# Performance work log

Measured on AMD Instinct MI355X. Metric: run time of the kernel, lower is better.

## Reference

```python
import jax, jax.numpy as jnp
import numpy as np

NUM_HEADS = 8
KEY_DIM = 32      # head_dim * attention_ratio = 64 * 0.5
HEAD_DIM = 64     # in_channels // num_heads = 512 // 8
SCALE = KEY_DIM ** -0.5


def _bn(y, g, b):
    # eval-mode BatchNorm2d with running_mean=0, running_var=1 -> per-channel affine
    return y * g[:, None, None] + b[:, None, None]


def setup_inputs() -> dict:
    key = jax.random.key(0)
    ks = jax.random.split(key, 4)
    B, C, H, W = 16, 512, 32, 32
    qkv_ch = C + 2 * NUM_HEADS * KEY_DIM  # 1024
    return {
        "x": jax.random.normal(ks[0], (B, C, H, W), jnp.float32),
        "w_qkv": jax.random.normal(ks[1], (qkv_ch, C), jnp.float32) * 0.02,
        "g_qkv": jnp.ones((qkv_ch,), jnp.float32),
        "b_qkv": jnp.zeros((qkv_ch,), jnp.float32),
        "w_pos": jax.random.normal(ks[2], (C, 1, 3, 3), jnp.float32) * 0.1,
        "g_pos": jnp.ones((C,), jnp.float32),
        "b_pos": jnp.zeros((C,), jnp.float32),
        "w_out": jax.random.normal(ks[3], (C, C), jnp.float32) * 0.02,
        "g_out": jnp.ones((C,), jnp.float32),
        "b_out": jnp.zeros((C,), jnp.float32),
    }


def reference(x, w_qkv, g_qkv, b_qkv, w_pos, g_pos, b_pos, w_out, g_out, b_out):
    B, C, H, W = x.shape
    HW = H * W
    # 1x1 conv QKV projection + BN (no activation)
    qkv = _bn(jnp.einsum('bchw,oc->bohw', x, w_qkv), g_qkv, b_qkv)
    # b (heads * (2*kd + hd)) h w -> b heads (2*kd + hd) hw
    qkv = qkv.reshape(B, NUM_HEADS, 2 * KEY_DIM + HEAD_DIM, HW)
    q = qkv[:, :, :KEY_DIM]                      # [B, h, kd, HW]
    k = qkv[:, :, KEY_DIM:2 * KEY_DIM]           # [B, h, kd, HW]
    v = qkv[:, :, 2 * KEY_DIM:]                  # [B, h, hd, HW]
    # attention scores: q^T k, scaled
    scores = jnp.einsum('bhdn,bhdm->bhnm', q, k) * SCALE   # [B, h, HW, HW]
    weights = jax.nn.softmax(scores, axis=-1)
    # attended = v @ weights^T : [B, h, hd, HW]
    attended = jnp.einsum('bhdm,bhnm->bhdn', v, weights)
    attended = attended.reshape(B, C, H, W)
    # positional encoding: depthwise 3x3 conv on value, + BN
    v_spatial = v.reshape(B, C, H, W)
    pos = jax.lax.conv_general_dilated(
        v_spatial, w_pos, window_strides=(1, 1), padding='SAME',
        feature_group_count=C, dimension_numbers=('NCHW', 'OIHW', 'NCHW'))
    pos = _bn(pos, g_pos, b_pos)
    enhanced = attended + pos
    # 1x1 output projection + BN
    return _bn(jnp.einsum('bchw,oc->bohw', enhanced, w_out), g_out, b_out)
```

## Files before the change

### kernel.cpp

```cpp
#include <hip/hip_runtime.h>
#include <hip/hip_bf16.h>
#include <stdint.h>

#define NHEADS 8
#define KDIM   32
#define HDIM   64
#define CDIM   512
#define HWN    1024
#define BATCH  16
#define QKVCH  1024
#define SCALE_F 0.17677669529663687f
#define QSCALE_F (0.17677669529663687f * 1.44269504088896341f)

typedef __attribute__((ext_vector_type(8))) short short8;
typedef __attribute__((ext_vector_type(4))) float f32x4;

static __device__ __forceinline__ unsigned short f2bf(float f) {
    unsigned int u = __float_as_uint(f);
    unsigned int r = (u + 0x7fffu + ((u >> 16) & 1u)) >> 16;
    return (unsigned short)r;
}
static __device__ __forceinline__ float bf2f(unsigned short h) {
    return __uint_as_float(((unsigned int)h) << 16);
}
static __device__ __forceinline__ unsigned int cvtpk(float a, float b) {
    unsigned int r;
    asm("v_cvt_pk_bf16_f32 %0, %1, %2" : "=v"(r) : "v"(a), "v"(b));
    return r;
}
static __device__ __forceinline__ float fexp2(float x) {
    float r;
    asm("v_exp_f32 %0, %1" : "=v"(r) : "v"(x));
    return r;
}
static __device__ __forceinline__ float bfelem(const uint4& v, int j) {
    unsigned int w = ((j >> 1) == 0) ? v.x : ((j >> 1) == 1) ? v.y : ((j >> 1) == 2) ? v.z : v.w;
    return (j & 1) ? __uint_as_float(w & 0xffff0000u) : __uint_as_float(w << 16);
}
static __device__ __forceinline__ unsigned int addpk(unsigned int a, unsigned int p) {
    float lo = __uint_as_float(a << 16) + __uint_as_float(p << 16);
    float hi = __uint_as_float(a & 0xffff0000u) + __uint_as_float(p & 0xffff0000u);
    return cvtpk(lo, hi);
}

static __device__ __forceinline__ void gload_lds16(const void* g, void* l) {
    __builtin_amdgcn_global_load_lds(
        (const __attribute__((address_space(1))) void*)g,
        (__attribute__((address_space(3))) void*)l, 16, 0, 0);
}

__global__ __launch_bounds__(256) void convert_kernel(const float* __restrict__ src,
                                                      unsigned short* __restrict__ dst, int n) {
    int i = (blockIdx.x * 256 + threadIdx.x) * 8;
    if (i >= n) return;
    float4 a = *(const float4*)(src + i);
    float4 c = *(const float4*)(src + i + 4);
    unsigned short r[8] __attribute__((aligned(16))) =
        {f2bf(a.x), f2bf(a.y), f2bf(a.z), f2bf(a.w), f2bf(c.x), f2bf(c.y), f2bf(c.z), f2bf(c.w)};
    *(uint4*)(dst + i) = *(const uint4*)r;
}

__global__ __launch_bounds__(256) void transpose_kernel(const float* __restrict__ x,
                                                        unsigned short* __restrict__ xt) {
    __shared__ unsigned short tl[64][66];
    int bid = blockIdx.x;
    int b = bid >> 7, ct = (bid >> 4) & 7, nt = bid & 15;
    int t = threadIdx.x;
#pragma unroll
    for (int i = 0; i < 16; ++i) {
        int idx = i * 256 + t;
        int cl = idx >> 6, nl = idx & 63;
        tl[cl][nl] = f2bf(x[((size_t)(b * CDIM + ct * 64 + cl)) * HWN + nt * 64 + nl]);
    }
    __syncthreads();
    int a8 = (t & 7) * 8;
    int nl = t >> 3;
#pragma unroll
    for (int i = 0; i < 2; ++i) {
        int n = nt * 64 + nl + 32 * i;
        unsigned short tmp[8] __attribute__((aligned(16)));
#pragma unroll
        for (int j = 0; j < 8; ++j) tmp[j] = tl[a8 + j][nl + 32 * i];
        *(uint4*)(xt + ((size_t)b * HWN + n) * CDIM + ct * 64 + a8) = *(const uint4*)tmp;
    }
}

template <int MODE>
__global__ __launch_bounds__(256) void gemm_bf16(
    const unsigned short* __restrict__ A, const unsigned short* __restrict__ Bt,
    const float* __restrict__ gvec, const float* __restrict__ bvec,
    void* out0, void* out1, void* out2, int Mtiles) {
    __shared__ unsigned short lds[2][128][32];
    int bid = blockIdx.x;
    int b  = bid / (Mtiles * 8);
    int rmn = bid % (Mtiles * 8);
    int mt = rmn >> 3, nt = rmn & 7;
    int t = threadIdx.x, lane = t & 63, w = t >> 6, g = lane >> 4, lr = lane & 15;
    int M0 = mt * 128, N0 = nt * 128;
    const unsigned short* Ab = A + (size_t)M0 * 512;
    const unsigned short* Bb = Bt + (size_t)b * HWN * 512 + (size_t)N0 * 512;
    int rw = (w >> 1) * 64, cw = (w & 1) * 64;

    f32x4 acc[4][4] = {};
    for (int k0 = 0; k0 < 512; k0 += 32) {
#pragma unroll
        for (int p = 0; p < 2; ++p) {
            int row = (p * 4 + w) * 16 + lr;
            int slot = lane >> 4;
            gload_lds16(Ab + row * 512 + k0 + slot * 8,
                        (char*)&lds[0][0][0] + (p * 4 + w) * 1024);
            gload_lds16(Bb + row * 512 + k0 + slot * 8,
                        (char*)&lds[1][0][0] + (p * 4 + w) * 1024);
        }
        __syncthreads();
        const char* Abase = (const char*)&lds[0][0][0] + lane * 16;
        const char* Bbase = (const char*)&lds[1][0][0] + lane * 16;
        short8 af[4], bfr[4];
#pragma unroll
        for (int i = 0; i < 4; ++i) {
            af[i]  = *(const short8*)(Abase + ((rw >> 4) + i) * 1024);
            bfr[i] = *(const short8*)(Bbase + ((cw >> 4) + i) * 1024);
        }
#pragma unroll
        for (int i = 0; i < 4; ++i)
#pragma unroll
            for (int j = 0; j < 4; ++j)
                acc[i][j] = __builtin_amdgcn_mfma_f32_16x16x32_bf16(af[i], bfr[j], acc[i][j], 0, 0, 0);
        __syncthreads();
    }

#pragma unroll
    for (int i = 0; i < 4; ++i) {
        int obase = M0 + rw + i * 16 + g * 4;
#pragma unroll
        for (int j = 0; j < 4; ++j) {
            int n = N0 + cw + j * 16 + lr;
            float val[4];
#pragma unroll
            for (int rr = 0; rr < 4; ++rr) {
                int o = obase + rr;
                val[rr] = acc[i][j][rr] * gvec[o] + bvec[o];
            }
            if (MODE == 0) {
                int h = obase >> 7, jj = obase & 127;
                size_t bh = (size_t)((b << 3) + h);
                if (jj < 32) {
                    uint2 pk = {cvtpk(val[0] * QSCALE_F, val[1] * QSCALE_F),
                                cvtpk(val[2] * QSCALE_F, val[3] * QSCALE_F)};
                    *(uint2*)((unsigned short*)out0 + (bh * HWN + n) * KDIM + jj) = pk;
                } else if (jj < 64) {
                    uint2 pk = {cvtpk(val[0], val[1]), cvtpk(val[2], val[3])};
                    *(uint2*)((unsigned short*)out1 + (bh * HWN + n) * KDIM + (jj - 32)) = pk;
                } else {
#pragma unroll
                    for (int rr = 0; rr < 4; ++rr)
                        ((unsigned short*)out2)[(bh * HDIM + (jj - 64 + rr)) * HWN + n] = f2bf(val[rr]);
                }
            } else {
#pragma unroll
                for (int rr = 0; rr < 4; ++rr)
                    ((float*)out0)[((size_t)(b * CDIM + obase + rr)) * HWN + n] = val[rr];
            }
        }
    }
}

__global__ __launch_bounds__(256) void attn_kernel(
    const unsigned short* __restrict__ qw, const unsigned short* __restrict__ kw,
    const unsigned short* __restrict__ vw, unsigned short* __restrict__ attw) {
    __shared__ unsigned short kt[2][128 * 32];
    __shared__ unsigned short vt[2][64 * 128];
    int p = blockIdx.x;
    int bh = ((p >> 6) << 3) | (p & 7);
    int ntile = (p >> 3) & 7;
    int b = bh >> 3, h = bh & 7;
    int t = threadIdx.x, lane = t & 63, w = t >> 6, g = lane >> 4, lr = lane & 15;
    int N0 = ntile * 128 + w * 32;
    const unsigned short* qb = qw + (size_t)bh * HWN * KDIM;
    const unsigned short* kb = kw + (size_t)bh * HWN * KDIM;
    const unsigned short* vb = vw + (size_t)bh * HDIM * HWN;

    short8 qf0 = *(const short8*)(qb + (size_t)(N0 + lr) * KDIM + g * 8);
    short8 qf1 = *(const short8*)(qb + (size_t)(N0 + 16 + lr) * KDIM + g * 8);
    f32x4 acc0[4] = {}, acc1[4] = {};
    f32x4 zero = {0.f, 0.f, 0.f, 0.f};
    float l0 = 0.f, l1 = 0.f;
    int sw = (lr & 7) << 4;
    int g8 = g << 3;

    auto stage = [&](int mt, int buf) {
        int M0 = mt * 128;
#pragma unroll
        for (int pp = 0; pp < 2; ++pp) {
            int s = pp * 256 + w * 64 + lane;
            int row = (s >> 7) * 32 + ((s >> 6) & 1) * 16 + lr;
            gload_lds16(kb + (size_t)(M0 + row) * KDIM + g * 8,
                        (char*)kt[buf] + (pp * 4 + w) * 1024);
        }
#pragma unroll
        for (int pp = 0; pp < 4; ++pp) {
            int s = pp * 256 + w * 64 + lane;
            int dd = s >> 4, u = s & 15;
            gload_lds16(vb + (size_t)dd * HWN + M0 + ((u ^ (dd & 7)) << 3),
                        (char*)vt[buf] + (pp * 4 + w) * 1024);
        }
    };

    stage(0, 0);
    __syncthreads();
    for (int mt = 0; mt < 8; ++mt) {
        int cur = mt & 1;
        if (mt < 7) stage(mt + 1, cur ^ 1);
        const char* ktc = (const char*)kt[cur] + lane * 16;
        const char* vrow = (const char*)vt[cur] + lr * 256;
#pragma unroll
        for (int mc = 0; mc < 4; ++mc) {
            short8 kf0 = *(const short8*)(ktc + mc * 2048);
            short8 kf1 = *(const short8*)(ktc + mc * 2048 + 1024);
            f32x4 s00 = __builtin_amdgcn_mfma_f32_16x16x32_bf16(kf0, qf0, zero, 0, 0, 0);
            f32x4 s01 = __builtin_amdgcn_mfma_f32_16x16x32_bf16(kf1, qf0, zero, 0, 0, 0);
            f32x4 s10 = __builtin_amdgcn_mfma_f32_16x16x32_bf16(kf0, qf1, zero, 0, 0, 0);
            f32x4 s11 = __builtin_amdgcn_mfma_f32_16x16x32_bf16(kf1, qf1, zero, 0, 0, 0);
            float e0[8], e1[8];
#pragma unroll
            for (int i = 0; i < 4; ++i) {
                e0[i] = fexp2(s00[i]); e0[4 + i] = fexp2(s01[i]);
                e1[i] = fexp2(s10[i]); e1[4 + i] = fexp2(s11[i]);
            }
            l0 += ((e0[0] + e0[1]) + (e0[2] + e0[3])) + ((e0[4] + e0[5]) + (e0[6] + e0[7]));
            l1 += ((e1[0] + e1[1]) + (e1[2] + e1[3])) + ((e1[4] + e1[5]) + (e1[6] + e1[7]));
            union { uint4 u; short8 s; } pf0, pf1;
            pf0.u = (uint4){cvtpk(e0[0], e0[1]), cvtpk(e0[2], e0[3]),
                            cvtpk(e0[4], e0[5]), cvtpk(e0[6], e0[7])};
            pf1.u = (uint4){cvtpk(e1[0], e1[1]), cvtpk(e1[2], e1[3]),
                            cvtpk(e1[4], e1[5]), cvtpk(e1[6], e1[7])};
            int off0 = (mc * 64 + g8) ^ sw;
            int off1 = off0 ^ 32;
#pragma unroll
            for (int dt = 0; dt < 4; ++dt) {
                uint2 v0 = *(const uint2*)(vrow + dt * 4096 + off0);
                uint2 v1 = *(const uint2*)(vrow + dt * 4096 + off1);
                union { uint2 u[2]; short8 s; } vf;
                vf.u[0] = v0; vf.u[1] = v1;
                acc0[dt] = __builtin_amdgcn_mfma_f32_16x16x32_bf16(vf.s, pf0.s, acc0[dt], 0, 0, 0);
                acc1[dt] = __builtin_amdgcn_mfma_f32_16x16x32_bf16(vf.s, pf1.s, acc1[dt], 0, 0, 0);
            }
        }
        __syncthreads();
    }
    l0 += __shfl_xor(l0, 16); l0 += __shfl_xor(l0, 32);
    l1 += __shfl_xor(l1, 16); l1 += __shfl_xor(l1, 32);
    float inv0 = 1.0f / l0, inv1 = 1.0f / l1;
    size_t robase = ((size_t)b * HWN + N0 + lr) * CDIM + h * HDIM + g * 4;
#pragma unroll
    for (int dt = 0; dt < 4; ++dt) {
        uint2 o0 = {cvtpk(acc0[dt][0] * inv0, acc0[dt][1] * inv0),
                    cvtpk(acc0[dt][2] * inv0, acc0[dt][3] * inv0)};
        uint2 o1 = {cvtpk(acc1[dt][0] * inv1, acc1[dt][1] * inv1),
                    cvtpk(acc1[dt][2] * inv1, acc1[dt][3] * inv1)};
        *(uint2*)(attw + robase + dt * 16) = o0;
        *(uint2*)(attw + robase + 16 * CDIM + dt * 16) = o1;
    }
}

__global__ __launch_bounds__(256) void conv_kernel(
    const unsigned short* __restrict__ vw,
    const float* __restrict__ wpos, const float* __restrict__ gpos, const float* __restrict__ bpos,
    const unsigned short* __restrict__ attw,
    unsigned short* __restrict__ ew) {
    __shared__ unsigned short po[32][520];
    int bid = blockIdx.x;
    int b = bid >> 5, y = bid & 31;
    int t = threadIdx.x;
#pragma unroll
    for (int hh = 0; hh < 2; ++hh) {
        int c = hh * 256 + t;
        const unsigned short* vrow = vw + ((size_t)(b * CDIM + c)) * HWN;
        uint4 rv[3][4];
#pragma unroll
        for (int dy = 0; dy < 3; ++dy) {
            int r = y + dy - 1;
            bool ok = (r >= 0) && (r < 32);
#pragma unroll
            for (int s2 = 0; s2 < 4; ++s2) {
                uint4 z = {0u, 0u, 0u, 0u};
                rv[dy][s2] = ok ? *(const uint4*)(vrow + r * 32 + s2 * 8) : z;
            }
        }
        float wreg[9];
#pragma unroll
        for (int k = 0; k < 9; ++k) wreg[k] = wpos[c * 9 + k];
        float gc = gpos[c], bc = bpos[c];
#pragma unroll
        for (int x = 0; x < 32; ++x) {
            float sum = 0.f;
#pragma unroll
            for (int dy = 0; dy < 3; ++dy)
#pragma unroll
                for (int dx = 0; dx < 3; ++dx) {
                    int xx = x + dx - 1;
                    if (xx >= 0 && xx < 32)
                        sum += wreg[dy * 3 + dx] * bfelem(rv[dy][xx >> 3], xx & 7);
                }
            po[x][c] = f2bf(sum * gc + bc);
        }
    }
    __syncthreads();
    int c8 = (t & 63) * 8;
    int xg = t >> 6;
#pragma unroll
    for (int i = 0; i < 8; ++i) {
        int x = xg + i * 4;
        size_t nidx = ((size_t)b * HWN + y * 32 + x) * CDIM + c8;
        uint4 a = *(const uint4*)(attw + nidx);
        uint4 p = *(const uint4*)(&po[x][c8]);
        uint4 o = {addpk(a.x, p.x), addpk(a.y, p.y), addpk(a.z, p.z), addpk(a.w, p.w)};
        *(uint4*)(ew + nidx) = o;
    }
}

extern "C" void kernel_launch(void* const* d_in, const int* in_sizes, int n_in,
                              void* d_out, int out_size, void* d_ws, size_t ws_size,
                              hipStream_t stream) {
    const float* x     = (const float*)d_in[0];
    const float* w_qkv = (const float*)d_in[1];
    const float* g_qkv = (const float*)d_in[2];
    const float* b_qkv = (const float*)d_in[3];
    const float* w_pos = (const float*)d_in[4];
    const float* g_pos = (const float*)d_in[5];
    const float* b_pos = (const float*)d_in[6];
    const float* w_out = (const float*)d_in[7];
    const float* g_out = (const float*)d_in[8];
    const float* b_out = (const float*)d_in[9];
    char* ws = (char*)d_ws;
    unsigned short* xt   = (unsigned short*)(ws);
    unsigned short* wqb  = (unsigned short*)(ws + 16777216);
    unsigned short* wob  = (unsigned short*)(ws + 17825792);
    unsigned short* qw   = (unsigned short*)(ws + 18350080);
    unsigned short* kw   = (unsigned short*)(ws + 26738688);
    unsigned short* vw   = (unsigned short*)(ws + 35127296);
    unsigned short* attw = (unsigned short*)(ws + 51904512);

    convert_kernel<<<256, 256, 0, stream>>>(w_qkv, wqb, QKVCH * CDIM);
    convert_kernel<<<128, 256, 0, stream>>>(w_out, wob, CDIM * CDIM);
    transpose_kernel<<<2048, 256, 0, stream>>>(x, xt);
    gemm_bf16<0><<<1024, 256, 0, stream>>>(wqb, xt, g_qkv, b_qkv, qw, kw, vw, 8);
    attn_kernel<<<1024, 256, 0, stream>>>(qw, kw, vw, attw);
    conv_kernel<<<512, 256, 0, stream>>>(vw, w_pos, g_pos, b_pos, attw, xt );
    gemm_bf16<1><<<512, 256, 0, stream>>>(wob, xt , g_out, b_out, d_out, nullptr, nullptr, 4);
}
```

Before: 162.5 us.

## Load GEMM fragments directly from global with register double-buffering and XCD-aware block mapping

After: 194.0 us. 1.19x slower.

```diff
diff --git a/kernel.cpp b/kernel.cpp
--- a/kernel.cpp
+++ b/kernel.cpp
@@ -85,48 +85,59 @@
     }
 }
 
-template <int MODE>
+template <int MODE, int MT>
 __global__ __launch_bounds__(256) void gemm_bf16(
     const unsigned short* __restrict__ A, const unsigned short* __restrict__ Bt,
     const float* __restrict__ gvec, const float* __restrict__ bvec,
-    void* out0, void* out1, void* out2, int Mtiles) {
-    __shared__ unsigned short lds[2][128][32];
-    int bid = blockIdx.x;
-    int b  = bid / (Mtiles * 8);
-    int rmn = bid % (Mtiles * 8);
-    int mt = rmn >> 3, nt = rmn & 7;
+    void* out0, void* out1, void* out2) {
+    constexpr int BPB = MT * 8;
+    int p = blockIdx.x;
+    int xcd = p & 7;
+    int r = p >> 3;
+    int hi = (r >= BPB) ? 1 : 0;
+    int b = xcd * 2 + hi;
+    int idx = r - hi * BPB;
+    int mt = idx >> 3, nt = idx & 7;
     int t = threadIdx.x, lane = t & 63, w = t >> 6, g = lane >> 4, lr = lane & 15;
     int M0 = mt * 128, N0 = nt * 128;
-    const unsigned short* Ab = A + (size_t)M0 * 512;
-    const unsigned short* Bb = Bt + (size_t)b * HWN * 512 + (size_t)N0 * 512;
     int rw = (w >> 1) * 64, cw = (w & 1) * 64;
 
+    const unsigned short* Ap = A + (size_t)(M0 + rw + lr) * 512 + g * 8;
+    const unsigned short* Bp = Bt + (size_t)b * HWN * 512 + (size_t)(N0 + cw + lr) * 512 + g * 8;
+
     f32x4 acc[4][4] = {};
-    for (int k0 = 0; k0 < 512; k0 += 32) {
-#pragma unroll
-        for (int p = 0; p < 2; ++p) {
-            int row = (p * 4 + w) * 16 + lr;
-            int slot = lane >> 4;
-            gload_lds16(Ab + row * 512 + k0 + slot * 8,
-                        (char*)&lds[0][0][0] + (p * 4 + w) * 1024);
-            gload_lds16(Bb + row * 512 + k0 + slot * 8,
-                        (char*)&lds[1][0][0] + (p * 4 + w) * 1024);
-        }
-        __syncthreads();
-        const char* Abase = (const char*)&lds[0][0][0] + lane * 16;
-        const char* Bbase = (const char*)&lds[1][0][0] + lane * 16;
-        short8 af[4], bfr[4];
-#pragma unroll
-        for (int i = 0; i < 4; ++i) {
-            af[i]  = *(const short8*)(Abase + ((rw >> 4) + i) * 1024);
-            bfr[i] = *(const short8*)(Bbase + ((cw >> 4) + i) * 1024);
+    short8 a0[4], b0[4], a1[4], b1[4];
+#pragma unroll
+    for (int i = 0; i < 4; ++i) {
+        a0[i] = *(const short8*)(Ap + i * 8192);
+        b0[i] = *(const short8*)(Bp + i * 8192);
+    }
+#pragma unroll
+    for (int ks = 0; ks < 16; ks += 2) {
+        if (ks + 1 < 16) {
+#pragma unroll
+            for (int i = 0; i < 4; ++i) {
+                a1[i] = *(const short8*)(Ap + i * 8192 + (ks + 1) * 32);
+                b1[i] = *(const short8*)(Bp + i * 8192 + (ks + 1) * 32);
+            }
         }
 #pragma unroll
         for (int i = 0; i < 4; ++i)
 #pragma unroll
             for (int j = 0; j < 4; ++j)
-                acc[i][j] = __builtin_amdgcn_mfma_f32_16x16x32_bf16(af[i], bfr[j], acc[i][j], 0, 0, 0);
-        __syncthreads();
+                acc[i][j] = __builtin_amdgcn_mfma_f32_16x16x32_bf16(a0[i], b0[j], acc[i][j], 0, 0, 0);
+        if (ks + 2 < 16) {
+#pragma unroll
+            for (int i = 0; i < 4; ++i) {
+                a0[i] = *(const short8*)(Ap + i * 8192 + (ks + 2) * 32);
+                b0[i] = *(const short8*)(Bp + i * 8192 + (ks + 2) * 32);
+            }
+        }
+#pragma unroll
+        for (int i = 0; i < 4; ++i)
+#pragma unroll
+            for (int j = 0; j < 4; ++j)
+                acc[i][j] = __builtin_amdgcn_mfma_f32_16x16x32_bf16(a1[i], b1[j], acc[i][j], 0, 0, 0);
     }
 
 #pragma unroll
@@ -344,8 +355,8 @@
     convert_kernel<<<256, 256, 0, stream>>>(w_qkv, wqb, QKVCH * CDIM);
     convert_kernel<<<128, 256, 0, stream>>>(w_out, wob, CDIM * CDIM);
     transpose_kernel<<<2048, 256, 0, stream>>>(x, xt);
-    gemm_bf16<0><<<1024, 256, 0, stream>>>(wqb, xt, g_qkv, b_qkv, qw, kw, vw, 8);
+    gemm_bf16<0, 8><<<1024, 256, 0, stream>>>(wqb, xt, g_qkv, b_qkv, qw, kw, vw);
     attn_kernel<<<1024, 256, 0, stream>>>(qw, kw, vw, attw);
     conv_kernel<<<512, 256, 0, stream>>>(vw, w_pos, g_pos, b_pos, attw, xt );
-    gemm_bf16<1><<<512, 256, 0, stream>>>(wob, xt , g_out, b_out, d_out, nullptr, nullptr, 4);
-}
+    gemm_bf16<1, 4><<<512, 256, 0, stream>>>(wob, xt , g_out, b_out, d_out, nullptr, nullptr);
+}
```

## Enlarge GEMM tiles, double-buffer LDS with K=64 stages, and XCD-aware block mapping

Applied to the files above, without the earlier changes.

After: 141.7 us. 1.15x faster.

```diff
diff --git a/kernel.cpp b/kernel.cpp
--- a/kernel.cpp
+++ b/kernel.cpp
@@ -85,56 +85,84 @@
     }
 }
 
-template <int MODE>
-__global__ __launch_bounds__(256) void gemm_bf16(
+template <int MODE, int BN, int WM, int WN, int NTB>
+__global__ __launch_bounds__(512, 2) void gemm_bf16(
     const unsigned short* __restrict__ A, const unsigned short* __restrict__ Bt,
     const float* __restrict__ gvec, const float* __restrict__ bvec,
-    void* out0, void* out1, void* out2, int Mtiles) {
-    __shared__ unsigned short lds[2][128][32];
-    int bid = blockIdx.x;
-    int b  = bid / (Mtiles * 8);
-    int rmn = bid % (Mtiles * 8);
-    int mt = rmn >> 3, nt = rmn & 7;
+    void* out0, void* out1, void* out2) {
+    constexpr int MF = 256 / (16 * WM);
+    constexpr int NF = BN / (16 * WN);
+    constexpr int BUFE = (256 + BN) * 64;
+    constexpr int BUNITS = BN * 8 / 512;
+    constexpr int PHB = BN * 4;
+    __shared__ unsigned short lds[2][BUFE];
+
+    int p = blockIdx.x;
+    int xcd = p & 7;
+    int j2 = p >> 3;
+    int b = xcd * 2 + (j2 >= 16 ? 1 : 0);
+    int idx = j2 & 15;
+    int mt = idx / NTB, ntl = idx % NTB;
     int t = threadIdx.x, lane = t & 63, w = t >> 6, g = lane >> 4, lr = lane & 15;
-    int M0 = mt * 128, N0 = nt * 128;
+    int M0 = mt * 256, N0 = ntl * BN;
+    int wr = (w / WN) * (16 * MF), wc = (w % WN) * (16 * NF);
+
     const unsigned short* Ab = A + (size_t)M0 * 512;
     const unsigned short* Bb = Bt + (size_t)b * HWN * 512 + (size_t)N0 * 512;
-    int rw = (w >> 1) * 64, cw = (w & 1) * 64;
-
-    f32x4 acc[4][4] = {};
-    for (int k0 = 0; k0 < 512; k0 += 32) {
-#pragma unroll
-        for (int p = 0; p < 2; ++p) {
-            int row = (p * 4 + w) * 16 + lr;
-            int slot = lane >> 4;
-            gload_lds16(Ab + row * 512 + k0 + slot * 8,
-                        (char*)&lds[0][0][0] + (p * 4 + w) * 1024);
-            gload_lds16(Bb + row * 512 + k0 + slot * 8,
-                        (char*)&lds[1][0][0] + (p * 4 + w) * 1024);
+
+    auto stage = [&](int kt, int buf) {
+        unsigned short* base = &lds[buf][0];
+#pragma unroll
+        for (int i = 0; i < 4; ++i) {
+            int U0 = i * 512 + w * 64;
+            int U = U0 + lane;
+            int h = U >> 10, rem = U & 1023;
+            int row = ((rem >> 6) << 4) + (lane & 15);
+            int k = ((lane >> 4) << 3) + (h << 5);
+            gload_lds16(Ab + (size_t)row * 512 + kt * 64 + k, (char*)base + U0 * 16);
+        }
+#pragma unroll
+        for (int i = 0; i < BUNITS; ++i) {
+            int U0 = i * 512 + w * 64;
+            int U = U0 + lane;
+            int h = U / PHB, rem = U % PHB;
+            int row = ((rem >> 6) << 4) + (lane & 15);
+            int k = ((lane >> 4) << 3) + (h << 5);
+            gload_lds16(Bb + (size_t)row * 512 + kt * 64 + k, (char*)base + 32768 + U0 * 16);
+        }
+    };
+
+    f32x4 acc[MF][NF] = {};
+    stage(0, 0);
+    __syncthreads();
+    for (int kt = 0; kt < 8; ++kt) {
+        int cur = kt & 1;
+        if (kt < 7) stage(kt + 1, cur ^ 1);
+        const unsigned short* base = &lds[cur][0];
+#pragma unroll
+        for (int h = 0; h < 2; ++h) {
+            short8 af[MF], bfr[NF];
+#pragma unroll
+            for (int i = 0; i < MF; ++i)
+                af[i] = *(const short8*)(base + h * 8192 + (((wr >> 4) + i) * 64 + lane) * 8);
+#pragma unroll
+            for (int j = 0; j < NF; ++j)
+                bfr[j] = *(const short8*)(base + 16384 + h * (BN * 32) + (((wc >> 4) + j) * 64 + lane) * 8);
+#pragma unroll
+            for (int i = 0; i < MF; ++i)
+#pragma unroll
+                for (int j = 0; j < NF; ++j)
+                    acc[i][j] = __builtin_amdgcn_mfma_f32_16x16x32_bf16(af[i], bfr[j], acc[i][j], 0, 0, 0);
         }
         __syncthreads();
-        const char* Abase = (const char*)&lds[0][0][0] + lane * 16;
-        const char* Bbase = (const char*)&lds[1][0][0] + lane * 16;
-        short8 af[4], bfr[4];
-#pragma unroll
-        for (int i = 0; i < 4; ++i) {
-            af[i]  = *(const short8*)(Abase + ((rw >> 4) + i) * 1024);
-            bfr[i] = *(const short8*)(Bbase + ((cw >> 4) + i) * 1024);
-        }
-#pragma unroll
-        for (int i = 0; i < 4; ++i)
-#pragma unroll
-            for (int j = 0; j < 4; ++j)
-                acc[i][j] = __builtin_amdgcn_mfma_f32_16x16x32_bf16(af[i], bfr[j], acc[i][j], 0, 0, 0);
-        __syncthreads();
-    }
-
-#pragma unroll
-    for (int i = 0; i < 4; ++i) {
-        int obase = M0 + rw + i * 16 + g * 4;
-#pragma unroll
-        for (int j = 0; j < 4; ++j) {
-            int n = N0 + cw + j * 16 + lr;
+    }
+
+#pragma unroll
+    for (int i = 0; i < MF; ++i) {
+        int obase = M0 + wr + i * 16 + g * 4;
+#pragma unroll
+        for (int j = 0; j < NF; ++j) {
+            int n = N0 + wc + j * 16 + lr;
             float val[4];
 #pragma unroll
             for (int rr = 0; rr < 4; ++rr) {
@@ -344,8 +372,8 @@
     convert_kernel<<<256, 256, 0, stream>>>(w_qkv, wqb, QKVCH * CDIM);
     convert_kernel<<<128, 256, 0, stream>>>(w_out, wob, CDIM * CDIM);
     transpose_kernel<<<2048, 256, 0, stream>>>(x, xt);
-    gemm_bf16<0><<<1024, 256, 0, stream>>>(wqb, xt, g_qkv, b_qkv, qw, kw, vw, 8);
+    gemm_bf16<0, 256, 2, 4, 4><<<256, 512, 0, stream>>>(wqb, xt, g_qkv, b_qkv, qw, kw, vw);
     attn_kernel<<<1024, 256, 0, stream>>>(qw, kw, vw, attw);
     conv_kernel<<<512, 256, 0, stream>>>(vw, w_pos, g_pos, b_pos, attw, xt );
-    gemm_bf16<1><<<512, 256, 0, stream>>>(wob, xt , g_out, b_out, d_out, nullptr, nullptr, 4);
-}
+    gemm_bf16<1, 128, 4, 2, 8><<<256, 512, 0, stream>>>(wob, xt , g_out, b_out, d_out, nullptr, nullptr);
+}
```
